# Kernel tuning notes

Measured on AMD Instinct MI355X. Metric: run time of the kernel, lower is better.

Reference implementation:

```python
import jax, jax.numpy as jnp
import numpy as np

ENC_DIM = 640
DEC_DIM = 640
INNER = 512
VOCAB = 2048


def setup_inputs() -> dict:
    key = jax.random.key(0)
    k1, k2, k3, k4, k5, k6 = jax.random.split(key, 6)
    B, T, U = 4, 256, 64
    enc_state = jax.random.normal(k1, (B, T, ENC_DIM), dtype=jnp.float32)
    dec_state = jax.random.normal(k2, (B, U, DEC_DIM), dtype=jnp.float32)
    s1 = 1.0 / np.sqrt(ENC_DIM + DEC_DIM)
    s2 = 1.0 / np.sqrt(INNER)
    W1 = jax.random.uniform(k3, (INNER, ENC_DIM + DEC_DIM), jnp.float32, -s1, s1)
    b1 = jax.random.uniform(k4, (INNER,), jnp.float32, -s1, s1)
    W2 = jax.random.uniform(k5, (VOCAB, INNER), jnp.float32, -s2, s2)
    b2 = jax.random.uniform(k6, (VOCAB,), jnp.float32, -s2, s2)
    return {"enc_state": enc_state, "dec_state": dec_state,
            "W1": W1, "b1": b1, "W2": W2, "b2": b2}


def reference(enc_state, dec_state, W1, b1, W2, b2):
    # Linear over concat([enc, dec]) == enc @ W_e^T + dec @ W_d^T (split weight),
    # applied over the broadcast T x U grid without materializing the concat tensor.
    We = W1[:, :ENC_DIM]   # [inner, enc_dim]
    Wd = W1[:, ENC_DIM:]   # [inner, dec_dim]
    enc_proj = jnp.einsum('bte,ie->bti', enc_state, We)  # [B,T,inner]
    dec_proj = jnp.einsum('bud,id->bui', dec_state, Wd)  # [B,U,inner]
    h = jnp.tanh(enc_proj[:, :, None, :] + dec_proj[:, None, :, :] + b1)  # [B,T,U,inner]
    logits = jnp.einsum('btui,vi->btuv', h, W2) + b2  # [B,T,U,vocab]
    return logits
```

## Files before the change

### kernel.cpp

```cpp
#include <hip/hip_runtime.h>
#include <hip/hip_bf16.h>
#include <cstdint>
#include <cstddef>


typedef __attribute__((ext_vector_type(8))) short   short8;
typedef __attribute__((ext_vector_type(4))) float   floatx4;

__device__ __forceinline__ short f2bf(float f) {
  union { float f; unsigned u; } v; v.f = f;
  unsigned r = (v.u + 0x7fffu + ((v.u >> 16) & 1u)) >> 16;
  return (short)(unsigned short)r;
}

__device__ __forceinline__ void async16(const void* g, void* l) {
  __builtin_amdgcn_global_load_lds(
      (const __attribute__((address_space(1))) unsigned int*)g,
      (__attribute__((address_space(3))) unsigned int*)l,
      16, 0, 0);
}

__global__ __launch_bounds__(256)
void f32_to_bf16(const float* __restrict__ in, short* __restrict__ out, int n8)
{
  const int i = blockIdx.x * 256 + threadIdx.x;
  if (i >= n8) return;
  const float4* p = (const float4*)in + 2 * (size_t)i;
  const float4 a = p[0], b = p[1];
  short8 o;
  o[0] = f2bf(a.x); o[1] = f2bf(a.y); o[2] = f2bf(a.z); o[3] = f2bf(a.w);
  o[4] = f2bf(b.x); o[5] = f2bf(b.y); o[6] = f2bf(b.z); o[7] = f2bf(b.w);
  ((short8*)out)[i] = o;
}

#define BUFB 49152

__global__ __launch_bounds__(512, 2)
void gemm_pipe(const short* __restrict__ A, int lda,
               const short* __restrict__ B, int ldb, int bcol,
               float* __restrict__ Cout, int ldc,
               const float* __restrict__ bias, int K, int nbx_sh)
{
  extern __shared__ char lds[];
  const int tid  = threadIdx.x;
  const int lane = tid & 63;
  const int w    = tid >> 6;
  const int wm   = (w >> 2) << 6;
  const int wn   = (w & 3) << 6;

  const int nwg = gridDim.x;
  const int qq = nwg >> 3, rr = nwg & 7;
  const int xcd = blockIdx.x & 7, idx = blockIdx.x >> 3;
  const int wg = (xcd < rr ? xcd * (qq + 1) : rr * (qq + 1) + (xcd - rr) * qq) + idx;
  const int nbx_mask = (1 << nbx_sh) - 1;
  const int m_base = (wg >> nbx_sh) << 7;
  const int n_base = (wg & nbx_mask) << 8;

  const int srow = tid >> 3;
  const int sblk = (tid & 7) ^ (srow & 7);
  const short* Asrc = A + (size_t)(m_base + srow) * lda + (sblk << 3);
  const short* Bsrc = B + (size_t)(n_base + srow) * ldb + bcol + (sblk << 3);
  const size_t a64 = (size_t)64 * lda;
  const size_t b64 = (size_t)64 * ldb;
  char* const ldst = lds + tid * 16;

  const int arow = lane & 15;
  const int q4   = lane >> 4;
  const int s7   = arow & 7;
  const int koff0 = ((q4)     ^ s7) << 4;
  const int koff1 = ((q4 + 4) ^ s7) << 4;
  const size_t aoff = (size_t)(wm + arow) * 128;
  const size_t boff = 16384 + (size_t)(wn + arow) * 128;

  floatx4 acc[4][4];
#pragma unroll
  for (int i = 0; i < 4; i++)
#pragma unroll
    for (int j = 0; j < 4; j++) acc[i][j] = (floatx4)0.0f;

  const int NT = K >> 6;

#pragma unroll
  for (int t = 0; t < 2; ++t) {
    const int kb = t << 6;
    char* dA = ldst + t * BUFB;
    char* dB = dA + 16384;
    async16(Asrc + kb,             dA);
    async16(Asrc + kb + a64,       dA + 8192);
    async16(Bsrc + kb,             dB);
    async16(Bsrc + kb + b64,       dB + 8192);
    async16(Bsrc + kb + 2 * b64,   dB + 16384);
    async16(Bsrc + kb + 3 * b64,   dB + 24576);
  }

  int r = 0;
  for (int kt = 0; kt < NT; ++kt) {
    if (kt + 1 < NT) asm volatile("s_waitcnt vmcnt(6)" ::: "memory");
    else             asm volatile("s_waitcnt vmcnt(0)" ::: "memory");
    __builtin_amdgcn_s_barrier();
    asm volatile("" ::: "memory");

    const char* Ab = lds + r * BUFB + aoff;
    const char* Bb = lds + r * BUFB + boff;
    const int r2 = (r >= 1) ? r - 1 : 2;
    char* dA = ldst + r2 * BUFB;
    char* dB = dA + 16384;
    const int  kb2 = (kt + 2) << 6;
    const bool do_stage = (kt + 2 < NT);

    short8 af[4], bf[4];

#pragma unroll
    for (int i = 0; i < 4; i++) af[i] = *(const short8*)(Ab + i * 2048 + koff0);
#pragma unroll
    for (int j = 0; j < 4; j++) bf[j] = *(const short8*)(Bb + j * 2048 + koff0);
    if (do_stage) {
      async16(Asrc + kb2,           dA);
      async16(Asrc + kb2 + a64,     dA + 8192);
      async16(Bsrc + kb2,           dB);
    }
    __builtin_amdgcn_s_barrier();
    asm volatile("s_waitcnt lgkmcnt(0)" ::: "memory");
    __builtin_amdgcn_s_setprio(1);
#pragma unroll
    for (int i = 0; i < 4; i++)
#pragma unroll
      for (int j = 0; j < 4; j++)
        acc[i][j] = __builtin_amdgcn_mfma_f32_16x16x32_bf16(af[i], bf[j], acc[i][j], 0, 0, 0);
    __builtin_amdgcn_s_setprio(0);

#pragma unroll
    for (int i = 0; i < 4; i++) af[i] = *(const short8*)(Ab + i * 2048 + koff1);
#pragma unroll
    for (int j = 0; j < 4; j++) bf[j] = *(const short8*)(Bb + j * 2048 + koff1);
    if (do_stage) {
      async16(Bsrc + kb2 + b64,     dB + 8192);
      async16(Bsrc + kb2 + 2 * b64, dB + 16384);
      async16(Bsrc + kb2 + 3 * b64, dB + 24576);
    }
    __builtin_amdgcn_s_barrier();
    asm volatile("s_waitcnt lgkmcnt(0)" ::: "memory");
    __builtin_amdgcn_s_setprio(1);
#pragma unroll
    for (int i = 0; i < 4; i++)
#pragma unroll
      for (int j = 0; j < 4; j++)
        acc[i][j] = __builtin_amdgcn_mfma_f32_16x16x32_bf16(af[i], bf[j], acc[i][j], 0, 0, 0);
    __builtin_amdgcn_s_setprio(0);

    r = (r == 2) ? 0 : r + 1;
  }

  const int quad = lane >> 4;
  const int coll = lane & 15;
  float bv[4] = {0.f, 0.f, 0.f, 0.f};
  if (bias) {
#pragma unroll
    for (int j = 0; j < 4; j++) bv[j] = bias[n_base + wn + j * 16 + coll];
  }
#pragma unroll
  for (int i = 0; i < 4; i++) {
#pragma unroll
    for (int rr2 = 0; rr2 < 4; rr2++) {
      const size_t row = (size_t)(m_base + wm + i * 16 + quad * 4 + rr2);
#pragma unroll
      for (int j = 0; j < 4; j++) {
        const size_t off = row * (size_t)ldc + (n_base + wn + j * 16 + coll);
        Cout[off] = acc[i][j][rr2] + bv[j];
      }
    }
  }
}

__global__ __launch_bounds__(256)
void tanh_fuse(const float* __restrict__ Pe, const float* __restrict__ Pd,
               const float* __restrict__ b1, short* __restrict__ H, int m0)
{
  const int idx = blockIdx.x * 256 + threadIdx.x;
  const int lm = idx >> 6;
  const int c = (idx & 63) << 3;
  const int m = m0 + lm;
  const int b = m >> 14;
  const int t = (m >> 6) & 255;
  const int u = m & 63;

  const float* pe = Pe + (size_t)((b << 8) + t) * 512 + c;
  const float* pd = Pd + (size_t)((b << 6) + u) * 512 + c;
  const float4 e0 = *(const float4*)pe;
  const float4 e1 = *(const float4*)(pe + 4);
  const float4 d0 = *(const float4*)pd;
  const float4 d1 = *(const float4*)(pd + 4);
  const float4 g0 = *(const float4*)(b1 + c);
  const float4 g1 = *(const float4*)(b1 + c + 4);

  float x[8] = {e0.x + d0.x + g0.x, e0.y + d0.y + g0.y,
                e0.z + d0.z + g0.z, e0.w + d0.w + g0.w,
                e1.x + d1.x + g1.x, e1.y + d1.y + g1.y,
                e1.z + d1.z + g1.z, e1.w + d1.w + g1.w};
  short8 o;
#pragma unroll
  for (int j = 0; j < 8; j++) {
    const float e  = __expf(2.0f * x[j]);
    const float th = 1.0f - 2.0f / (e + 1.0f);
    o[j] = f2bf(th);
  }
  *(short8*)(H + (size_t)lm * 512 + c) = o;
}

extern "C" void kernel_launch(void* const* d_in, const int* in_sizes, int n_in,
                              void* d_out, int out_size, void* d_ws, size_t ws_size,
                              hipStream_t stream)
{
  const float* enc = (const float*)d_in[0];
  const float* dec = (const float*)d_in[1];
  const float* W1  = (const float*)d_in[2];
  const float* b1  = (const float*)d_in[3];
  const float* W2  = (const float*)d_in[4];
  const float* b2  = (const float*)d_in[5];
  float* out = (float*)d_out;

  static bool attr_done = false;
  if (!attr_done) {
    hipFuncSetAttribute((const void*)gemm_pipe,
                        hipFuncAttributeMaxDynamicSharedMemorySize, 3 * BUFB);
    attr_done = true;
  }

  size_t off = 0;
  auto carve = [&](size_t bytes) -> void* {
    void* p = (char*)d_ws + off;
    off += (bytes + 255) & ~(size_t)255;
    return p;
  };
  short* encb = (short*)carve(1024 * 640 * 2);
  short* decb = (short*)carve(256 * 640 * 2);
  short* W1b  = (short*)carve(512 * 1280 * 2);
  short* W2b  = (short*)carve(2048 * 512 * 2);
  float* Pe   = (float*)carve(1024 * 512 * 4);
  float* Pd   = (float*)carve(256 * 512 * 4);
  short* H    = (short*)((char*)d_ws + off);

  const size_t avail = (ws_size > off) ? (ws_size - off) : 0;
  long long rpc = (long long)(avail / (512 * 2));
  rpc = (rpc / 128) * 128;
  if (rpc < 128) rpc = 128;
  if (rpc > 65536) rpc = 65536;

  auto cgrid = [](int n8) { return (unsigned)((n8 + 255) / 256); };
  const int n8_enc = 1024 * 640 / 8;
  const int n8_dec = 256 * 640 / 8;
  const int n8_W1  = 512 * 1280 / 8;
  const int n8_W2  = 2048 * 512 / 8;
  f32_to_bf16<<<cgrid(n8_enc), 256, 0, stream>>>(enc, encb, n8_enc);
  f32_to_bf16<<<cgrid(n8_dec), 256, 0, stream>>>(dec, decb, n8_dec);
  f32_to_bf16<<<cgrid(n8_W1),  256, 0, stream>>>(W1,  W1b,  n8_W1);
  f32_to_bf16<<<cgrid(n8_W2),  256, 0, stream>>>(W2,  W2b,  n8_W2);

  gemm_pipe<<<16, 512, 3 * BUFB, stream>>>(encb, 640, W1b, 1280, 0,
                                           Pe, 512, nullptr, 640, 1);
  gemm_pipe<<<4, 512, 3 * BUFB, stream>>>(decb, 640, W1b, 1280, 640,
                                          Pd, 512, nullptr, 640, 1);

  for (long long m0 = 0; m0 < 65536; m0 += rpc) {
    const long long rows = (65536 - m0 < rpc) ? (65536 - m0) : rpc;
    tanh_fuse<<<(unsigned)(rows / 4), 256, 0, stream>>>(Pe, Pd, b1, H, (int)m0);
    gemm_pipe<<<(unsigned)(8 * (rows / 128)), 512, 3 * BUFB, stream>>>(
        H, 512, W2b, 512, 0, out + (size_t)m0 * 2048, 2048, b2, 512, 3);
  }
}
```

Measured before the change: 714.2 us.

## Fuse tanh activation into output GEMM, keeping H tile resident in LDS

Replaces the separate tanh kernel plus chunked output GEMM with one kernel per 128-row M tile. Each tile computes tanh(Pe+Pd+b1) straight into swizzled LDS as bf16, then streams W2 across all 8 N tiles with double-buffered async loads. This removes the global write and read of the 65536x512 H matrix and the chunked launches. The four cast kernels are also merged into one launch. In exchange, each block uses 160KB of LDS, which limits occupancy to one block per CU. The grid of 512 blocks relies on that single-block occupancy being enough to hide latency.

```diff
diff --git a/kernel.cpp b/kernel.cpp
--- a/kernel.cpp
+++ b/kernel.cpp
@@ -1,5 +1,4 @@
 #include <hip/hip_runtime.h>
-#include <hip/hip_bf16.h>
 #include <cstdint>
 #include <cstddef>
 
@@ -21,16 +20,23 @@
 }
 
 __global__ __launch_bounds__(256)
-void f32_to_bf16(const float* __restrict__ in, short* __restrict__ out, int n8)
+void cast_all(const float* __restrict__ enc, const float* __restrict__ dec,
+              const float* __restrict__ W1,  const float* __restrict__ W2,
+              short* __restrict__ encb, short* __restrict__ decb,
+              short* __restrict__ W1b,  short* __restrict__ W2b)
 {
   const int i = blockIdx.x * 256 + threadIdx.x;
-  if (i >= n8) return;
-  const float4* p = (const float4*)in + 2 * (size_t)i;
+  const float* in; short* out; int j;
+  if (i < 81920)       { in = enc; out = encb; j = i; }
+  else if (i < 102400) { in = dec; out = decb; j = i - 81920; }
+  else if (i < 184320) { in = W1;  out = W1b;  j = i - 102400; }
+  else                 { in = W2;  out = W2b;  j = i - 184320; }
+  const float4* p = (const float4*)in + 2 * (size_t)j;
   const float4 a = p[0], b = p[1];
   short8 o;
   o[0] = f2bf(a.x); o[1] = f2bf(a.y); o[2] = f2bf(a.z); o[3] = f2bf(a.w);
   o[4] = f2bf(b.x); o[5] = f2bf(b.y); o[6] = f2bf(b.z); o[7] = f2bf(b.w);
-  ((short8*)out)[i] = o;
+  ((short8*)out)[j] = o;
 }
 
 #define BUFB 49152
@@ -172,39 +178,148 @@
   }
 }
 
-__global__ __launch_bounds__(256)
-void tanh_fuse(const float* __restrict__ Pe, const float* __restrict__ Pd,
-               const float* __restrict__ b1, short* __restrict__ H, int m0)
-{
-  const int idx = blockIdx.x * 256 + threadIdx.x;
-  const int lm = idx >> 6;
-  const int c = (idx & 63) << 3;
-  const int m = m0 + lm;
-  const int b = m >> 14;
-  const int t = (m >> 6) & 255;
-  const int u = m & 63;
-
-  const float* pe = Pe + (size_t)((b << 8) + t) * 512 + c;
-  const float* pd = Pd + (size_t)((b << 6) + u) * 512 + c;
-  const float4 e0 = *(const float4*)pe;
-  const float4 e1 = *(const float4*)(pe + 4);
-  const float4 d0 = *(const float4*)pd;
-  const float4 d1 = *(const float4*)(pd + 4);
-  const float4 g0 = *(const float4*)(b1 + c);
-  const float4 g1 = *(const float4*)(b1 + c + 4);
-
-  float x[8] = {e0.x + d0.x + g0.x, e0.y + d0.y + g0.y,
-                e0.z + d0.z + g0.z, e0.w + d0.w + g0.w,
-                e1.x + d1.x + g1.x, e1.y + d1.y + g1.y,
-                e1.z + d1.z + g1.z, e1.w + d1.w + g1.w};
-  short8 o;
-#pragma unroll
-  for (int j = 0; j < 8; j++) {
-    const float e  = __expf(2.0f * x[j]);
-    const float th = 1.0f - 2.0f / (e + 1.0f);
-    o[j] = f2bf(th);
-  }
-  *(short8*)(H + (size_t)lm * 512 + c) = o;
+__device__ __forceinline__ void store_tile(float* __restrict__ out,
+    const float* __restrict__ b2, floatx4 (&acc)[4][4],
+    int m_base, int nt, int wm, int wn, int lane)
+{
+  const int quad = lane >> 4;
+  const int coll = lane & 15;
+  const int ncol0 = nt * 256 + wn + coll;
+  float bv[4];
+#pragma unroll
+  for (int j = 0; j < 4; j++) bv[j] = b2[ncol0 + j * 16];
+#pragma unroll
+  for (int i = 0; i < 4; i++) {
+#pragma unroll
+    for (int r = 0; r < 4; r++) {
+      const size_t row = (size_t)(m_base + wm + i * 16 + quad * 4 + r);
+      float* o = out + row * 2048 + ncol0;
+#pragma unroll
+      for (int j = 0; j < 4; j++) o[j * 16] = acc[i][j][r] + bv[j];
+    }
+  }
+}
+
+__global__ __launch_bounds__(512, 2)
+void joint_fused(const float* __restrict__ Pe, const float* __restrict__ Pd,
+                 const float* __restrict__ b1, const short* __restrict__ W2b,
+                 const float* __restrict__ b2, float* __restrict__ out)
+{
+  extern __shared__ char lds[];
+  short* Hs = (short*)lds;
+  char*  Wb0 = lds + 131072;
+
+  const int tid  = threadIdx.x;
+  const int lane = tid & 63;
+  const int w    = tid >> 6;
+  const int wm   = (w >> 2) << 6;
+  const int wn   = (w & 3) << 6;
+  const int m_base = blockIdx.x << 7;
+  const int b  = m_base >> 14;
+  const int t0 = (m_base >> 6) & 255;
+
+  const short* w2base = W2b + ((size_t)(tid >> 2) * 512) + ((tid & 3) << 3);
+  char* const wdst = Wb0 + tid * 16;
+
+  async16(w2base,             wdst);
+  async16(w2base + 128 * 512, wdst + 8192);
+
+  {
+    const int hrow = tid >> 2;
+    const int cseg = (tid & 3) << 7;
+    const float* pe = Pe + (size_t)((b << 8) + t0 + (hrow >> 6)) * 512 + cseg;
+    const float* pd = Pd + (size_t)((b << 6) + (hrow & 63)) * 512 + cseg;
+    const float* bb = b1 + cseg;
+    short* hrowp = Hs + (size_t)hrow * 512;
+    const int sw = hrow & 7;
+#pragma unroll 4
+    for (int j = 0; j < 16; ++j) {
+      const float4 e0 = *(const float4*)(pe + j * 8);
+      const float4 e1 = *(const float4*)(pe + j * 8 + 4);
+      const float4 d0 = *(const float4*)(pd + j * 8);
+      const float4 d1 = *(const float4*)(pd + j * 8 + 4);
+      const float4 g0 = *(const float4*)(bb + j * 8);
+      const float4 g1 = *(const float4*)(bb + j * 8 + 4);
+      float x[8] = {e0.x + d0.x + g0.x, e0.y + d0.y + g0.y,
+                    e0.z + d0.z + g0.z, e0.w + d0.w + g0.w,
+                    e1.x + d1.x + g1.x, e1.y + d1.y + g1.y,
+                    e1.z + d1.z + g1.z, e1.w + d1.w + g1.w};
+      short8 o;
+#pragma unroll
+      for (int q = 0; q < 8; q++) {
+        const float e  = __expf(2.0f * x[q]);
+        const float th = 1.0f - 2.0f / (e + 1.0f);
+        o[q] = f2bf(th);
+      }
+      const int blk = (cseg >> 3) + j;
+      *(short8*)(hrowp + (((blk ^ sw)) << 3)) = o;
+    }
+  }
+  __syncthreads();
+
+  const int arow = lane & 15;
+  const int q4   = lane >> 4;
+  const int s7   = arow & 7;
+  const char* HsB = (const char*)lds;
+  size_t abase[4];
+#pragma unroll
+  for (int i = 0; i < 4; i++) abase[i] = (size_t)(wm + i * 16 + arow) * 1024;
+  int boff[4];
+#pragma unroll
+  for (int j = 0; j < 4; j++) boff[j] = (wn + j * 16 + arow) * 64 + q4 * 16;
+
+  floatx4 acc[4][4];
+#pragma unroll
+  for (int i = 0; i < 4; i++)
+#pragma unroll
+    for (int j = 0; j < 4; j++) acc[i][j] = (floatx4)0.0f;
+
+#pragma unroll 2
+  for (int g = 0; g < 128; ++g) {
+    const int kt = g & 15;
+
+    if (g > 0) {
+      asm volatile("s_waitcnt vmcnt(0)" ::: "memory");
+      __builtin_amdgcn_s_barrier();
+      asm volatile("" ::: "memory");
+      if (kt == 0) {
+        store_tile(out, b2, acc, m_base, (g >> 4) - 1, wm, wn, lane);
+#pragma unroll
+        for (int i = 0; i < 4; i++)
+#pragma unroll
+          for (int j = 0; j < 4; j++) acc[i][j] = (floatx4)0.0f;
+      }
+    }
+
+    if (g + 1 < 128) {
+      const int nt1 = (g + 1) >> 4, kt1 = (g + 1) & 15;
+      const short* src = w2base + (size_t)(nt1 << 8) * 512 + (kt1 << 5);
+      char* dst = Wb0 + (((g + 1) & 1) << 14) + tid * 16;
+      async16(src,             dst);
+      async16(src + 128 * 512, dst + 8192);
+    }
+    asm volatile("" ::: "memory");
+
+    const char* wb = Wb0 + ((g & 1) << 14);
+    short8 af[4], bf[4];
+#pragma unroll
+    for (int i = 0; i < 4; i++) {
+      const int kb = ((kt << 2) | q4) ^ s7;
+      af[i] = *(const short8*)(HsB + abase[i] + (kb << 4));
+    }
+#pragma unroll
+    for (int j = 0; j < 4; j++) bf[j] = *(const short8*)(wb + boff[j]);
+
+    __builtin_amdgcn_s_setprio(1);
+#pragma unroll
+    for (int i = 0; i < 4; i++)
+#pragma unroll
+      for (int j = 0; j < 4; j++)
+        acc[i][j] = __builtin_amdgcn_mfma_f32_16x16x32_bf16(af[i], bf[j], acc[i][j], 0, 0, 0);
+    __builtin_amdgcn_s_setprio(0);
+  }
+
+  store_tile(out, b2, acc, m_base, 7, wm, wn, lane);
 }
 
 extern "C" void kernel_launch(void* const* d_in, const int* in_sizes, int n_in,
@@ -223,6 +338,8 @@
   if (!attr_done) {
     hipFuncSetAttribute((const void*)gemm_pipe,
                         hipFuncAttributeMaxDynamicSharedMemorySize, 3 * BUFB);
+    hipFuncSetAttribute((const void*)joint_fused,
+                        hipFuncAttributeMaxDynamicSharedMemorySize, 163840);
     attr_done = true;
   }
 
@@ -238,33 +355,13 @@
   short* W2b  = (short*)carve(2048 * 512 * 2);
   float* Pe   = (float*)carve(1024 * 512 * 4);
   float* Pd   = (float*)carve(256 * 512 * 4);
-  short* H    = (short*)((char*)d_ws + off);
-
-  const size_t avail = (ws_size > off) ? (ws_size - off) : 0;
-  long long rpc = (long long)(avail / (512 * 2));
-  rpc = (rpc / 128) * 128;
-  if (rpc < 128) rpc = 128;
-  if (rpc > 65536) rpc = 65536;
-
-  auto cgrid = [](int n8) { return (unsigned)((n8 + 255) / 256); };
-  const int n8_enc = 1024 * 640 / 8;
-  const int n8_dec = 256 * 640 / 8;
-  const int n8_W1  = 512 * 1280 / 8;
-  const int n8_W2  = 2048 * 512 / 8;
-  f32_to_bf16<<<cgrid(n8_enc), 256, 0, stream>>>(enc, encb, n8_enc);
-  f32_to_bf16<<<cgrid(n8_dec), 256, 0, stream>>>(dec, decb, n8_dec);
-  f32_to_bf16<<<cgrid(n8_W1),  256, 0, stream>>>(W1,  W1b,  n8_W1);
-  f32_to_bf16<<<cgrid(n8_W2),  256, 0, stream>>>(W2,  W2b,  n8_W2);
+
+  cast_all<<<1232, 256, 0, stream>>>(enc, dec, W1, W2, encb, decb, W1b, W2b);
 
   gemm_pipe<<<16, 512, 3 * BUFB, stream>>>(encb, 640, W1b, 1280, 0,
                                            Pe, 512, nullptr, 640, 1);
   gemm_pipe<<<4, 512, 3 * BUFB, stream>>>(decb, 640, W1b, 1280, 640,
                                           Pd, 512, nullptr, 640, 1);
 
-  for (long long m0 = 0; m0 < 65536; m0 += rpc) {
-    const long long rows = (65536 - m0 < rpc) ? (65536 - m0) : rpc;
-    tanh_fuse<<<(unsigned)(rows / 4), 256, 0, stream>>>(Pe, Pd, b1, H, (int)m0);
-    gemm_pipe<<<(unsigned)(8 * (rows / 128)), 512, 3 * BUFB, stream>>>(
-        H, 512, W2b, 512, 0, out + (size_t)m0 * 2048, 2048, b2, 512, 3);
-  }
-}
+  joint_fused<<<512, 512, 163840, stream>>>(Pe, Pd, b1, W2b, b2, out);
+}
```

New measurement: 718.1 us. No clear change (+0.6%).
